# Kernel tuning notes

Measured on AMD Instinct MI355X. Metric: run time of the kernel, lower is better.

The kernel has to match this reference:

```python
import jax, jax.numpy as jnp
import numpy as np

NUM_HEADS = 8
NUM_KV_HEADS = 2
PATCH = 16
STRIDE = 8
HORIZON = 96
NQ = 3
EPS_RMS = 1e-6
EPS_REVIN = 1e-5


def rms_norm(x, scale):
    return x * jax.lax.rsqrt(jnp.mean(x * x, axis=-1, keepdims=True) + EPS_RMS) * scale


def lstm_scan(xs, wi, wh, b):
    # xs: (N, T, Din); flax OptimizedLSTMCell gate order i, f, g, o
    N = xs.shape[0]
    H = wh.shape[0]

    def step(carry, x_t):
        c, h = carry
        z = x_t @ wi + h @ wh + b
        i, f, g, o = jnp.split(z, 4, axis=-1)
        c = jax.nn.sigmoid(f) * c + jax.nn.sigmoid(i) * jnp.tanh(g)
        h = jax.nn.sigmoid(o) * jnp.tanh(c)
        return (c, h), h

    init = (jnp.zeros((N, H), xs.dtype), jnp.zeros((N, H), xs.dtype))
    _, hs = jax.lax.scan(step, init, jnp.swapaxes(xs, 0, 1))
    return jnp.swapaxes(hs, 0, 1)  # (N, T, H)


def gqa(x, wq, wk, wv, wo):
    # x: (B, S, D); non-causal grouped-query attention
    B, S, D = x.shape
    hd = wq.shape[1] // NUM_HEADS
    q = (x @ wq).reshape(B, S, NUM_HEADS, hd)
    k = (x @ wk).reshape(B, S, NUM_KV_HEADS, hd)
    v = (x @ wv).reshape(B, S, NUM_KV_HEADS, hd)
    rep = NUM_HEADS // NUM_KV_HEADS
    k = jnp.repeat(k, rep, axis=2)
    v = jnp.repeat(v, rep, axis=2)
    scale = jnp.asarray(1.0 / np.sqrt(hd), x.dtype)
    attn = jax.nn.softmax(jnp.einsum('bqhd,bkhd->bhqk', q, k) * scale, axis=-1)
    out = jnp.einsum('bhqk,bkhd->bqhd', attn, v).reshape(B, S, NUM_HEADS * hd)
    return out @ wo, attn


def setup_inputs() -> dict:
    key = jax.random.key(0)
    ks = jax.random.split(key, 12)
    b, d, m, T = 8, 16, 8, 512
    H, H2 = 256, 512
    NB = 4

    def w(k, shape, fan_in):
        return jax.random.normal(k, shape, jnp.float32) / np.sqrt(fan_in)

    return {
        'series': jax.random.normal(ks[0], (b, d, m, T), jnp.float32),
        'revin_scale': jnp.ones((m,), jnp.float32),
        'revin_bias': jnp.zeros((m,), jnp.float32),
        'up_w': w(ks[1], (PATCH, H), PATCH),
        'lstm_wi': w(ks[2], (NB, H, 4 * H2), H),
        'lstm_wh': w(ks[3], (NB, H2, 4 * H2), H2),
        'lstm_b': jnp.zeros((NB, 4 * H2), jnp.float32),
        'norm_scale': jnp.ones((NB, H2), jnp.float32),
        'wq': w(ks[4], (NB, H2, H2), H2),
        'wk': w(ks[5], (NB, H2, H2 // 4), H2),
        'wv': w(ks[6], (NB, H2, H2 // 4), H2),
        'wo': w(ks[7], (NB, H2, H2), H2),
        'down_w': w(ks[8], (NB, H2, H), H2),
        'head_norm_scale': jnp.ones((H,), jnp.float32),
        'point_w': w(ks[9], (H, HORIZON), H),
        'quant_w': w(ks[10], (H, HORIZON * NQ), H),
    }


def reference(series, revin_scale, revin_bias, up_w, lstm_wi, lstm_wh, lstm_b,
              norm_scale, wq, wk, wv, wo, down_w, head_norm_scale, point_w, quant_w):
    b, d, m, T = series.shape
    num_blocks = lstm_wi.shape[0]
    H = up_w.shape[1]
    H2 = lstm_wh.shape[1]

    # RevIN instance norm over time with per-metric affine
    mean = series.mean(axis=-1, keepdims=True)
    std = jnp.sqrt(series.var(axis=-1, keepdims=True) + EPS_REVIN)
    sc = revin_scale[:, None]
    bi = revin_bias[:, None]
    normed = (series - mean) / std * sc + bi

    # Patcher (seq_len=512, patch=16, stride=8 -> 63 patches, no padding needed)
    n_p = (T - PATCH) // STRIDE + 1
    idx = jnp.arange(n_p)[:, None] * STRIDE + jnp.arange(PATCH)
    patches = normed[..., idx]            # (b, d, m, np, ps)
    x = patches @ up_w                    # (b, d, m, np, H)

    for blk in range(num_blocks):
        s = x.reshape(b * d * m, n_p, H)
        hs = lstm_scan(s, lstm_wi[blk], lstm_wh[blk], lstm_b[blk])  # (bdm, np, H2)
        # '(b d m) np h -> (b m np) d h'
        hs = hs.reshape(b, d, m, n_p, H2).transpose(0, 2, 3, 1, 4).reshape(b * m * n_p, d, H2)
        nrm = rms_norm(hs, norm_scale[blk])
        mix, _ = gqa(nrm, wq[blk], wk[blk], wv[blk], wo[blk])
        bel = mix @ down_w[blk]           # (bmnp, d, H)
        # '(b m np) d h -> b d m np h'
        x = bel.reshape(b, m, n_p, d, H).transpose(0, 3, 1, 2, 4)

    # pooling_mode == 'last' with device mixer: last block's belief at last patch
    last = x[:, :, :, -1, :]              # (b, d, m, H)
    nb = rms_norm(last, head_norm_scale)
    point = nb @ point_w                  # (b, d, m, horizon)
    quant = (nb @ quant_w).reshape(b, d, m, HORIZON, NQ).transpose(4, 0, 1, 2, 3)

    def denorm(y):
        return (y - bi) / sc * std + mean

    point_u = denorm(point)
    quant_u = denorm(quant)               # broadcasts over leading quantile axis
    return jnp.concatenate([point_u[None], quant_u], axis=0)  # (1+NQ, b, d, m, horizon)
```

## Files before the change

### kernel.cpp

```cpp
#include <hip/hip_runtime.h>
#include <hip/hip_bf16.h>

#define NP 63

typedef __attribute__((ext_vector_type(8))) short short8;
typedef __attribute__((ext_vector_type(4))) float f32x4;
typedef __attribute__((ext_vector_type(4))) int i32x4;
typedef unsigned char uchar;

__device__ __forceinline__ float sigf(float x){ return 1.0f/(1.0f+expf(-x)); }
__device__ __forceinline__ float u2f(ushort u){ __hip_bfloat16 h; *(ushort*)&h = u; return __bfloat162float(h); }
__device__ __forceinline__ ushort f2u(float f){ __hip_bfloat16 h = __float2bfloat16(f); return *(ushort*)&h; }

__global__ void __launch_bounds__(256) k_revin(const float* __restrict__ series,
    float* __restrict__ meanv, float* __restrict__ stdv, int* __restrict__ bar)
{
  int n = blockIdx.x, tid = threadIdx.x;
  if(n==0 && tid<64) bar[tid] = 0;
  __shared__ float s1[256], s2[256];
  const float* p = series + n*512;
  float a = 0.f, b = 0.f;
  for(int t=tid;t<512;t+=256){ float v=p[t]; a+=v; b+=v*v; }
  s1[tid]=a; s2[tid]=b; __syncthreads();
  for(int s=128;s>0;s>>=1){
    if(tid<s){ s1[tid]+=s1[tid+s]; s2[tid]+=s2[tid+s]; }
    __syncthreads();
  }
  if(tid==0){
    float mu = s1[0]*(1.f/512.f);
    float var = fmaxf(s2[0]*(1.f/512.f) - mu*mu, 0.f);
    meanv[n]=mu; stdv[n]=sqrtf(var+1e-5f);
  }
}

__global__ void __launch_bounds__(256) k_patch(const float* __restrict__ series,
    const float* __restrict__ rs, const float* __restrict__ rb,
    const float* __restrict__ up_w, const float* __restrict__ meanv,
    const float* __restrict__ stdv, ushort* __restrict__ x)
{
  int n = blockIdx.x, tid = threadIdx.x;
  int m = n & 7;
  __shared__ float sn[512];
  float mu = meanv[n], sd = stdv[n];
  float A = rs[m]/sd, C = rb[m] - mu*A;
  const float* p = series + n*512;
  for(int t=tid;t<512;t+=256) sn[t] = p[t]*A + C;
  __syncthreads();
  float w[16];
  #pragma unroll
  for(int i=0;i<16;i++) w[i] = up_w[i*256+tid];
  ushort* xo = x + n*(NP*256);
  for(int pi=0;pi<NP;pi++){
    float acc=0.f;
    #pragma unroll
    for(int i=0;i<16;i++) acc = fmaf(sn[pi*8+i], w[i], acc);
    xo[pi*256+tid] = f2u(acc);
  }
}

__global__ void __launch_bounds__(256) k_wod(const float* __restrict__ wo,
    const float* __restrict__ dw, float* __restrict__ wod)
{
  int i = blockIdx.x, blk = blockIdx.y, tid = threadIdx.x;
  __shared__ float row[512];
  const float* wr = wo + (blk*512 + i)*512;
  for(int k=tid;k<512;k+=256) row[k]=wr[k];
  __syncthreads();
  const float* d = dw + blk*512*256;
  float acc=0.f;
  for(int k=0;k<512;k++) acc = fmaf(row[k], d[k*256+tid], acc);
  wod[(blk*512+i)*256+tid]=acc;
}

__global__ void __launch_bounds__(256) k_tr_wodt(const float* __restrict__ wod, ushort* __restrict__ wodt)
{
  __shared__ float tile[32][33];
  int blk = blockIdx.z;
  int n0 = blockIdx.x*32, k0 = blockIdx.y*32;
  int tid = threadIdx.x;
  #pragma unroll
  for(int i=0;i<4;i++){
    int idx = tid + 256*i; int kl = idx>>5, nl = idx&31;
    tile[kl][nl] = wod[blk*512*256 + (k0+kl)*256 + n0+nl];
  }
  __syncthreads();
  #pragma unroll
  for(int i=0;i<4;i++){
    int idx = tid + 256*i; int nl = idx>>5, kl = idx&31;
    wodt[blk*256*512 + (n0+nl)*512 + k0+kl] = f2u(tile[kl][nl]);
  }
}

__global__ void __launch_bounds__(256) k_tr_lstmw(const float* __restrict__ wi,
    const float* __restrict__ wh, ushort* __restrict__ wt)
{
  __shared__ float tile[32][33];
  int blk = blockIdx.z;
  int n0 = blockIdx.x*32, k0 = blockIdx.y*32;
  int tid = threadIdx.x;
  #pragma unroll
  for(int i=0;i<4;i++){
    int idx = tid + 256*i; int kl = idx>>5, nl = idx&31;
    int k = k0+kl, n = n0+nl;
    float v = (k<256) ? wi[blk*256*2048 + k*2048 + n]
                      : wh[blk*512*2048 + (k-256)*2048 + n];
    tile[kl][nl] = v;
  }
  __syncthreads();
  #pragma unroll
  for(int i=0;i<4;i++){
    int idx = tid + 256*i; int nl = idx>>5, kl = idx&31;
    wt[blk*2048*768 + (n0+nl)*768 + k0+kl] = f2u(tile[kl][nl]);
  }
}

__global__ void __launch_bounds__(256) k_tr_qkvw(const float* __restrict__ wq,
    const float* __restrict__ wk, const float* __restrict__ wv,
    const float* __restrict__ ns, ushort* __restrict__ wqkvt)
{
  __shared__ float tile[32][33];
  int blk = blockIdx.z;
  int n0 = blockIdx.x*32, k0 = blockIdx.y*32;
  int tid = threadIdx.x;
  #pragma unroll
  for(int i=0;i<4;i++){
    int idx = tid + 256*i; int kl = idx>>5, nl = idx&31;
    int k = k0+kl, n = n0+nl;
    float v;
    if(n < 512)      v = wq[blk*512*512 + k*512 + n];
    else if(n < 640) v = wk[blk*512*128 + k*128 + (n-512)];
    else             v = wv[blk*512*128 + k*128 + (n-640)];
    tile[kl][nl] = v * ns[blk*512 + k];
  }
  __syncthreads();
  #pragma unroll
  for(int i=0;i<4;i++){
    int idx = tid + 256*i; int nl = idx>>5, kl = idx&31;
    wqkvt[blk*768*512 + (n0+nl)*512 + k0+kl] = f2u(tile[kl][nl]);
  }
}

__global__ void __launch_bounds__(256,1) k_lstm_scan(
    const ushort* __restrict__ x, ushort* __restrict__ hs,
    const ushort* __restrict__ wt, const float* __restrict__ bias,
    uchar* __restrict__ flags, int tagbase)
{
  __shared__ __align__(16) short Bwh[128*512];
  __shared__ __align__(16) ushort hstage[64*32];
  int fb = blockIdx.x;
  int g = (fb & 7) | ((fb >> 4) & 8);
  int y = (fb >> 3) & 15;
  int n0 = g*64, jj0 = y*32;
  int tid = threadIdx.x;
  int wv = tid>>6, lane = tid&63, quad = lane>>4, l16 = lane&15;
  int wrow = wv>>1, wcol = wv&1;

  for(int i=tid; i<8192; i+=256){
    int c = i>>6, kb = i&63;
    short8 v = *(const short8*)(wt + ((c>>5)*512 + jj0 + (c&31))*768 + 256 + kb*8);
    *(short8*)((char*)Bwh + c*1024 + ((kb*16) ^ ((c&7)<<4))) = v;
  }
  int jj = jj0 + wcol*16 + l16;
  short8 bwi[4][8];
  #pragma unroll
  for(int gg=0; gg<4; gg++){
    const ushort* wp = wt + (gg*512 + jj)*768 + quad*8;
    #pragma unroll
    for(int ck=0; ck<8; ck++) bwi[gg][ck] = *(const short8*)(wp + ck*32);
  }
  float bI=bias[jj], bF=bias[512+jj], bG=bias[1024+jj], bO=bias[1536+jj];
  float cs[2][4];
  #pragma unroll
  for(int a=0;a<2;a++){
    #pragma unroll
    for(int r=0;r<4;r++) cs[a][r]=0.f;
  }
  const ushort* xb0 = x  + (n0 + wrow*32 + l16)*(NP*256) + quad*8;
  const ushort* hb0 = hs + (n0 + wrow*32 + l16)*(NP*512) + quad*8;
  int xorb = (l16&7)<<4;
  uchar* myflag = flags + g*16 + y;
  const uchar* gflags = flags + g*16;
  __syncthreads();

  for(int t=0; t<NP; ++t){
    f32x4 acc[4][2];
    #pragma unroll
    for(int gg=0; gg<4; gg++){ acc[gg][0]=(f32x4){0.f,0.f,0.f,0.f}; acc[gg][1]=(f32x4){0.f,0.f,0.f,0.f}; }

    #pragma unroll
    for(int ck=0; ck<8; ck++){
      short8 a0 = *(const short8*)(xb0 + t*256 + ck*32);
      short8 a1 = *(const short8*)(xb0 + 16*(NP*256) + t*256 + ck*32);
      #pragma unroll
      for(int gg=0; gg<4; gg++){
        acc[gg][0] = __builtin_amdgcn_mfma_f32_16x16x32_bf16(a0, bwi[gg][ck], acc[gg][0], 0,0,0);
        acc[gg][1] = __builtin_amdgcn_mfma_f32_16x16x32_bf16(a1, bwi[gg][ck], acc[gg][1], 0,0,0);
      }
    }

    if(t > 0){
      if(tid==0){
        uint tag = (uint)(tagbase + t);
        while(1){
          i32x4 f;
          asm volatile("global_load_dwordx4 %0, %1, off sc0 sc1\n\ts_waitcnt vmcnt(0)"
                       : "=&v"(f) : "v"(gflags) : "memory");
          uint ok = 1u;
          #pragma unroll
          for(int q=0;q<4;q++){
            uint w = (uint)f[q];
            if(( w      &0xffu) < tag) ok=0;
            if(((w>>8 ) &0xffu) < tag) ok=0;
            if(((w>>16) &0xffu) < tag) ok=0;
            if( (w>>24)         < tag) ok=0;
          }
          if(ok) break;
          __builtin_amdgcn_s_sleep(1);
        }
      }
      __syncthreads();

      const ushort* hb = hb0 + (t-1)*512;
      #pragma unroll
      for(int ck=0; ck<16; ck++){
        short8 a0 = *(const short8*)(hb + ck*32);
        short8 a1 = *(const short8*)(hb + 16*(NP*512) + ck*32);
        #pragma unroll
        for(int gg=0; gg<4; gg++){
          int c = gg*32 + wcol*16 + l16;
          short8 bh = *(short8*)((char*)Bwh + c*1024 + ((ck*64 + quad*16) ^ xorb));
          acc[gg][0] = __builtin_amdgcn_mfma_f32_16x16x32_bf16(a0, bh, acc[gg][0], 0,0,0);
          acc[gg][1] = __builtin_amdgcn_mfma_f32_16x16x32_bf16(a1, bh, acc[gg][1], 0,0,0);
        }
      }
    }

    #pragma unroll
    for(int a=0;a<2;a++){
      #pragma unroll
      for(int r=0;r<4;r++){
        int rowl = wrow*32 + a*16 + quad*4 + r;
        float zi=acc[0][a][r]+bI, zf=acc[1][a][r]+bF, zg=acc[2][a][r]+bG, zo=acc[3][a][r]+bO;
        float c = sigf(zf)*cs[a][r] + sigf(zi)*tanhf(zg);
        cs[a][r] = c;
        float hv = sigf(zo)*tanhf(c);
        int coll = wcol*16 + l16;
        int off = rowl*64 + ((coll*2) ^ (((rowl>>2)&3)<<4));
        *(ushort*)((char*)hstage + off) = f2u(hv);
      }
    }
    __syncthreads();
    {
      int rowl = tid>>2, c0b = (tid&3)*16;
      int off = rowl*64 + (c0b ^ (((rowl>>2)&3)<<4));
      i32x4 vv = *(const i32x4*)((const char*)hstage + off);
      ushort* gp = hs + ((size_t)(n0+rowl)*NP + t)*512 + jj0 + (tid&3)*8;
      asm volatile("global_store_dwordx4 %0, %1, off sc0 sc1" :: "v"(gp), "v"(vv) : "memory");
    }
    __syncthreads();
    if(tid==0 && t < NP-1){
      uint v = (uint)(tagbase + t + 1);
      asm volatile("global_store_byte %0, %1, off sc0 sc1" :: "v"(myflag), "v"(v) : "memory");
    }
  }
}

__global__ void __launch_bounds__(256) k_rms(const ushort* __restrict__ hs, float* __restrict__ rmsi)
{
  int tid = threadIdx.x;
  int r = blockIdx.x*4 + (tid>>6);
  int lane = tid&63;
  int bq = r/8064; int rr = r - bq*8064;
  int m = rr/1008; int rem = rr - m*1008;
  int p = rem>>4; int d = rem&15;
  int n = (bq*16+d)*8+m;
  const ushort* hp = hs + (n*NP+p)*512;
  float s=0.f;
  for(int c=lane;c<512;c+=64){ float v=u2f(hp[c]); s += v*v; }
  #pragma unroll
  for(int off=32;off>0;off>>=1) s += __shfl_down(s,off);
  if(lane==0) rmsi[r] = rsqrtf(s*(1.f/512.f)+1e-6f);
}

__global__ void __launch_bounds__(256) k_qkv_m(
    const ushort* __restrict__ hs, const float* __restrict__ rmsi,
    const ushort* __restrict__ wqkvt, ushort* __restrict__ qkv)
{
  __shared__ short As[64*40];
  __shared__ short Bs[128*40];
  int tid = threadIdx.x;
  int r0 = blockIdx.x*64, c0 = blockIdx.y*128;
  int wv = tid>>6, lane = tid&63, quad = lane>>4, l16 = lane&15;
  int arow = tid>>2, akp = tid&3;
  int r = r0 + arow;
  int bq = r/8064; int rr = r - bq*8064;
  int m = rr/1008; int rem = rr - m*1008;
  int p = rem>>4; int d = rem&15;
  int n = (bq*16+d)*8+m;
  const ushort* aptr = hs + (n*NP+p)*512 + akp*8;
  f32x4 acc[2][4];
  #pragma unroll
  for(int b=0;b<2;b++){
    #pragma unroll
    for(int a=0;a<4;a++) acc[b][a] = (f32x4){0.f,0.f,0.f,0.f};
  }
  for(int k0=0;k0<512;k0+=32){
    *(short8*)&As[arow*40+akp*8] = *(const short8*)(aptr + k0);
    #pragma unroll
    for(int i=0;i<2;i++){
      int pc = tid + 256*i; int rl=pc>>2, kp=pc&3;
      *(short8*)&Bs[rl*40+kp*8] = *(const short8*)(wqkvt + (c0+rl)*512 + k0 + kp*8);
    }
    __syncthreads();
    short8 af[4], bfr[2];
    #pragma unroll
    for(int a=0;a<4;a++) af[a] = *(short8*)&As[(a*16+l16)*40 + quad*8];
    #pragma unroll
    for(int b=0;b<2;b++) bfr[b] = *(short8*)&Bs[(wv*32+b*16+l16)*40 + quad*8];
    #pragma unroll
    for(int b=0;b<2;b++){
      #pragma unroll
      for(int a=0;a<4;a++)
        acc[b][a] = __builtin_amdgcn_mfma_f32_16x16x32_bf16(af[a], bfr[b], acc[b][a], 0,0,0);
    }
    __syncthreads();
  }
  #pragma unroll
  for(int a=0;a<4;a++){
    #pragma unroll
    for(int rg=0;rg<4;rg++){
      int rw = r0 + a*16 + quad*4 + rg;
      float rv = rmsi[rw];
      #pragma unroll
      for(int b=0;b<2;b++){
        int c = c0 + wv*32 + b*16 + l16;
        qkv[rw*768 + c] = f2u(acc[b][a][rg] * rv);
      }
    }
  }
}

__global__ void __launch_bounds__(256) k_attn(ushort* __restrict__ qkv)
{
  int r3 = blockIdx.x, h = blockIdx.y;
  int tid = threadIdx.x;
  __shared__ float qs[16][64];
  __shared__ float ks[16][65];
  __shared__ float vs[16][64];
  __shared__ float P[16][17];
  ushort* base = qkv + r3*16*768;
  int xx = tid&63, s4 = tid>>6;
  int kvh = (h>>2)*64;
  #pragma unroll
  for(int a=0;a<4;a++){
    int s = s4 + 4*a;
    qs[s][xx] = u2f(base[s*768 + h*64 + xx]);
    ks[s][xx] = u2f(base[s*768 + 512 + kvh + xx]);
    vs[s][xx] = u2f(base[s*768 + 640 + kvh + xx]);
  }
  __syncthreads();
  int i = tid>>4, j = tid&15;
  float sc = 0.f;
  #pragma unroll
  for(int xq=0;xq<64;xq++) sc = fmaf(qs[i][xq], ks[j][xq], sc);
  P[i][j] = sc*0.125f;
  __syncthreads();
  float row[16];
  #pragma unroll
  for(int jj=0;jj<16;jj++) row[jj] = P[i][jj];
  float mx = row[0];
  #pragma unroll
  for(int jj=1;jj<16;jj++) mx = fmaxf(mx, row[jj]);
  float sum = 0.f;
  #pragma unroll
  for(int jj=0;jj<16;jj++) sum += expf(row[jj]-mx);
  float pme = expf(row[j]-mx)/sum;
  __syncthreads();
  P[i][j] = pme;
  __syncthreads();
  #pragma unroll
  for(int a=0;a<4;a++){
    int s = s4 + 4*a;
    float o = 0.f;
    #pragma unroll
    for(int jj=0;jj<16;jj++) o = fmaf(P[s][jj], vs[jj][xx], o);
    base[s*768 + h*64 + xx] = f2u(o);
  }
}

__global__ void __launch_bounds__(256) k_bel_m(
    const ushort* __restrict__ qkv, const ushort* __restrict__ wodt,
    ushort* __restrict__ x)
{
  __shared__ short As[64*40];
  __shared__ short Bs[128*40];
  int tid = threadIdx.x;
  int r0 = blockIdx.x*64, c0 = blockIdx.y*128;
  int wv = tid>>6, lane = tid&63, quad = lane>>4, l16 = lane&15;
  int arow = tid>>2, akp = tid&3;
  const ushort* aptr = qkv + (r0+arow)*768 + akp*8;
  f32x4 acc[2][4];
  #pragma unroll
  for(int b=0;b<2;b++){
    #pragma unroll
    for(int a=0;a<4;a++) acc[b][a] = (f32x4){0.f,0.f,0.f,0.f};
  }
  for(int k0=0;k0<512;k0+=32){
    *(short8*)&As[arow*40+akp*8] = *(const short8*)(aptr + k0);
    #pragma unroll
    for(int i=0;i<2;i++){
      int pc = tid + 256*i; int rl=pc>>2, kp=pc&3;
      *(short8*)&Bs[rl*40+kp*8] = *(const short8*)(wodt + (c0+rl)*512 + k0 + kp*8);
    }
    __syncthreads();
    short8 af[4], bfr[2];
    #pragma unroll
    for(int a=0;a<4;a++) af[a] = *(short8*)&As[(a*16+l16)*40 + quad*8];
    #pragma unroll
    for(int b=0;b<2;b++) bfr[b] = *(short8*)&Bs[(wv*32+b*16+l16)*40 + quad*8];
    #pragma unroll
    for(int b=0;b<2;b++){
      #pragma unroll
      for(int a=0;a<4;a++)
        acc[b][a] = __builtin_amdgcn_mfma_f32_16x16x32_bf16(af[a], bfr[b], acc[b][a], 0,0,0);
    }
    __syncthreads();
  }
  #pragma unroll
  for(int a=0;a<4;a++){
    #pragma unroll
    for(int rg=0;rg<4;rg++){
      int rw = r0 + a*16 + quad*4 + rg;
      int bq = rw/8064; int rr = rw - bq*8064;
      int m = rr/1008; int rem = rr - m*1008;
      int p = rem>>4; int d = rem&15;
      int n = (bq*16+d)*8+m;
      ushort* xo = x + (n*NP+p)*256;
      #pragma unroll
      for(int b=0;b<2;b++){
        int c = c0 + wv*32 + b*16 + l16;
        xo[c] = f2u(acc[b][a][rg]);
      }
    }
  }
}

__global__ void __launch_bounds__(256) k_head(const ushort* __restrict__ x,
    const float* __restrict__ meanv, const float* __restrict__ stdv,
    const float* __restrict__ rs, const float* __restrict__ rb,
    const float* __restrict__ hns, const float* __restrict__ pw,
    const float* __restrict__ qw, float* __restrict__ out)
{
  int n = blockIdx.x, tid = threadIdx.x;
  __shared__ float nb[256];
  __shared__ float red[256];
  float v = u2f(x[(n*NP + 62)*256 + tid]);
  red[tid] = v*v; __syncthreads();
  for(int s=128;s>0;s>>=1){
    if(tid<s) red[tid]+=red[tid+s];
    __syncthreads();
  }
  float rinv = rsqrtf(red[0]*(1.f/256.f)+1e-6f);
  nb[tid] = v*rinv*hns[tid];
  __syncthreads();
  int m = n&7;
  float mu=meanv[n], sd=stdv[n], sc=rs[m], bi=rb[m];
  for(int col=tid; col<384; col+=256){
    float acc=0.f;
    int slot, hh;
    if(col < 96){
      for(int k=0;k<256;k++) acc = fmaf(nb[k], pw[k*96+col], acc);
      slot = 0; hh = col;
    } else {
      int cq = col-96;
      for(int k=0;k<256;k++) acc = fmaf(nb[k], qw[k*288+cq], acc);
      int qi = cq - (cq/3)*3;
      slot = 1 + qi; hh = cq/3;
    }
    float y = (acc - bi)/sc*sd + mu;
    out[(slot*1024 + n)*96 + hh] = y;
  }
}

extern "C" void kernel_launch(void* const* d_in, const int* in_sizes, int n_in,
                              void* d_out, int out_size, void* d_ws, size_t ws_size,
                              hipStream_t stream)
{
  const float* series    = (const float*)d_in[0];
  const float* rs        = (const float*)d_in[1];
  const float* rb        = (const float*)d_in[2];
  const float* up_w      = (const float*)d_in[3];
  const float* lstm_wi   = (const float*)d_in[4];
  const float* lstm_wh   = (const float*)d_in[5];
  const float* lstm_b    = (const float*)d_in[6];
  const float* norm_scale= (const float*)d_in[7];
  const float* wq        = (const float*)d_in[8];
  const float* wk        = (const float*)d_in[9];
  const float* wv        = (const float*)d_in[10];
  const float* wo        = (const float*)d_in[11];
  const float* down_w    = (const float*)d_in[12];
  const float* head_ns   = (const float*)d_in[13];
  const float* point_w   = (const float*)d_in[14];
  const float* quant_w   = (const float*)d_in[15];
  float* out = (float*)d_out;

  float* ws = (float*)d_ws;
  float*  meanv = ws;
  float*  stdv  = meanv + 1024;
  float*  rmsi  = stdv  + 1024;
  float*  cst   = rmsi  + 64512;
  float*  wodf  = cst   + 524288;
  ushort* xbuf  = (ushort*)(wodf + 524288);
  ushort* hsb   = xbuf  + 16515072;
  ushort* qkvb  = hsb   + 33030144;
  ushort* wt    = qkvb  + 49545216;
  ushort* wqkvt = wt    + 6291456;
  ushort* wodt  = wqkvt + 1572864;
  int*    bar   = (int*)cst;

  k_revin<<<1024,256,0,stream>>>(series, meanv, stdv, bar);
  k_patch<<<1024,256,0,stream>>>(series, rs, rb, up_w, meanv, stdv, xbuf);
  k_wod<<<dim3(512,4),256,0,stream>>>(wo, down_w, wodf);
  k_tr_wodt<<<dim3(8,16,4),256,0,stream>>>(wodf, wodt);
  k_tr_lstmw<<<dim3(64,24,4),256,0,stream>>>(lstm_wi, lstm_wh, wt);
  k_tr_qkvw<<<dim3(24,16,4),256,0,stream>>>(wq, wk, wv, norm_scale, wqkvt);

  for(int blk=0; blk<4; blk++){
    const ushort* wt_b = wt + blk*2048*768;
    const float*  bb   = lstm_b + blk*2048;
    k_lstm_scan<<<256,256,0,stream>>>(xbuf, hsb, wt_b, bb, (uchar*)bar, blk*NP);
    k_rms<<<16128,256,0,stream>>>(hsb, rmsi);
    k_qkv_m<<<dim3(1008,6),256,0,stream>>>(hsb, rmsi, wqkvt + blk*768*512, qkvb);
    k_attn<<<dim3(4032,8),256,0,stream>>>(qkvb);
    k_bel_m<<<dim3(1008,2),256,0,stream>>>(qkvb, wodt + blk*256*512, xbuf);
  }
  k_head<<<1024,256,0,stream>>>(xbuf, meanv, stdv, rs, rb, head_ns, point_w, quant_w, out);
}
```

Before: 3.818 ms.

## Use per-wave progress flags and per-chunk waits in LSTM scan

Replaces the block-wide barrier and single-thread spin in the persistent LSTM scan with per-wavefront flags: every wave publishes its own step counter, loads the group's flags before the input matmul, and waits only on the producer of each 32-column h chunk before consuming it. The LDS staging buffer and the two syncthreads per step are removed, and h values are written directly as scattered 2-byte global stores. Each block now gets its own flag region, so no tag offset is needed. The intent is to cut cross-block synchronization latency on the serial recurrence, at the cost of many more, smaller uncoalesced stores and more polling traffic.

```diff
diff --git a/kernel.cpp b/kernel.cpp
--- a/kernel.cpp
+++ b/kernel.cpp
@@ -12,11 +12,16 @@
 __device__ __forceinline__ float u2f(ushort u){ __hip_bfloat16 h; *(ushort*)&h = u; return __bfloat162float(h); }
 __device__ __forceinline__ ushort f2u(float f){ __hip_bfloat16 h = __float2bfloat16(f); return *(ushort*)&h; }
 
+__device__ __forceinline__ bool bytes_ok(uint d, uint tag){
+  return ((d & 0xffu) >= tag) & (((d>>8) & 0xffu) >= tag) &
+         (((d>>16) & 0xffu) >= tag) & ((d>>24) >= tag);
+}
+
 __global__ void __launch_bounds__(256) k_revin(const float* __restrict__ series,
     float* __restrict__ meanv, float* __restrict__ stdv, int* __restrict__ bar)
 {
   int n = blockIdx.x, tid = threadIdx.x;
-  if(n==0 && tid<64) bar[tid] = 0;
+  if(n==0){ for(int i=tid;i<1024;i+=256) bar[i]=0; }
   __shared__ float s1[256], s2[256];
   const float* p = series + n*512;
   float a = 0.f, b = 0.f;
@@ -143,10 +148,9 @@
 __global__ void __launch_bounds__(256,1) k_lstm_scan(
     const ushort* __restrict__ x, ushort* __restrict__ hs,
     const ushort* __restrict__ wt, const float* __restrict__ bias,
-    uchar* __restrict__ flags, int tagbase)
+    uchar* __restrict__ flags)
 {
   __shared__ __align__(16) short Bwh[128*512];
-  __shared__ __align__(16) ushort hstage[64*32];
   int fb = blockIdx.x;
   int g = (fb & 7) | ((fb >> 4) & 8);
   int y = (fb >> 3) & 15;
@@ -178,11 +182,19 @@
   const ushort* xb0 = x  + (n0 + wrow*32 + l16)*(NP*256) + quad*8;
   const ushort* hb0 = hs + (n0 + wrow*32 + l16)*(NP*512) + quad*8;
   int xorb = (l16&7)<<4;
-  uchar* myflag = flags + g*16 + y;
-  const uchar* gflags = flags + g*16;
+  const uchar* gflags = flags + g*64;
+  uchar* myflag = flags + g*64 + y*4 + wv;
   __syncthreads();
 
   for(int t=0; t<NP; ++t){
+    i32x4 f0, f1, f2, f3;
+    if(t > 0){
+      asm volatile("global_load_dwordx4 %0, %1, off sc0 sc1" : "=&v"(f0) : "v"(gflags)    );
+      asm volatile("global_load_dwordx4 %0, %1, off sc0 sc1" : "=&v"(f1) : "v"(gflags+16) );
+      asm volatile("global_load_dwordx4 %0, %1, off sc0 sc1" : "=&v"(f2) : "v"(gflags+32) );
+      asm volatile("global_load_dwordx4 %0, %1, off sc0 sc1" : "=&v"(f3) : "v"(gflags+48) );
+    }
+
     f32x4 acc[4][2];
     #pragma unroll
     for(int gg=0; gg<4; gg++){ acc[gg][0]=(f32x4){0.f,0.f,0.f,0.f}; acc[gg][1]=(f32x4){0.f,0.f,0.f,0.f}; }
@@ -199,68 +211,58 @@
     }
 
     if(t > 0){
-      if(tid==0){
-        uint tag = (uint)(tagbase + t);
-        while(1){
-          i32x4 f;
-          asm volatile("global_load_dwordx4 %0, %1, off sc0 sc1\n\ts_waitcnt vmcnt(0)"
-                       : "=&v"(f) : "v"(gflags) : "memory");
-          uint ok = 1u;
+      asm volatile("s_waitcnt vmcnt(0)" : "+v"(f0), "+v"(f1), "+v"(f2), "+v"(f3) :: "memory");
+      const ushort* hb = hb0 + (t-1)*512;
+      uint tag = (uint)t;
+      #pragma unroll
+      for(int yy=0; yy<16; yy++){
+        uint d;
+        if(yy<4)       d = (uint)f0[yy&3];
+        else if(yy<8)  d = (uint)f1[yy&3];
+        else if(yy<12) d = (uint)f2[yy&3];
+        else           d = (uint)f3[yy&3];
+        if(!bytes_ok(d, tag)){
+          const uchar* qa = gflags + (yy>>2)*16;
+          i32x4 fr;
+          do {
+            __builtin_amdgcn_s_sleep(1);
+            asm volatile("global_load_dwordx4 %0, %1, off sc0 sc1\n\ts_waitcnt vmcnt(0)"
+                         : "=&v"(fr) : "v"(qa) : "memory");
+            d = (uint)fr[yy&3];
+          } while(!bytes_ok(d, tag));
+        }
+        {
+          const int ck = yy;
+          short8 a0 = *(const short8*)(hb + ck*32);
+          short8 a1 = *(const short8*)(hb + 16*(NP*512) + ck*32);
           #pragma unroll
-          for(int q=0;q<4;q++){
-            uint w = (uint)f[q];
-            if(( w      &0xffu) < tag) ok=0;
-            if(((w>>8 ) &0xffu) < tag) ok=0;
-            if(((w>>16) &0xffu) < tag) ok=0;
-            if( (w>>24)         < tag) ok=0;
+          for(int gg=0; gg<4; gg++){
+            int c = gg*32 + wcol*16 + l16;
+            short8 bh = *(short8*)((char*)Bwh + c*1024 + ((ck*64 + quad*16) ^ xorb));
+            acc[gg][0] = __builtin_amdgcn_mfma_f32_16x16x32_bf16(a0, bh, acc[gg][0], 0,0,0);
+            acc[gg][1] = __builtin_amdgcn_mfma_f32_16x16x32_bf16(a1, bh, acc[gg][1], 0,0,0);
           }
-          if(ok) break;
-          __builtin_amdgcn_s_sleep(1);
         }
       }
-      __syncthreads();
-
-      const ushort* hb = hb0 + (t-1)*512;
-      #pragma unroll
-      for(int ck=0; ck<16; ck++){
-        short8 a0 = *(const short8*)(hb + ck*32);
-        short8 a1 = *(const short8*)(hb + 16*(NP*512) + ck*32);
-        #pragma unroll
-        for(int gg=0; gg<4; gg++){
-          int c = gg*32 + wcol*16 + l16;
-          short8 bh = *(short8*)((char*)Bwh + c*1024 + ((ck*64 + quad*16) ^ xorb));
-          acc[gg][0] = __builtin_amdgcn_mfma_f32_16x16x32_bf16(a0, bh, acc[gg][0], 0,0,0);
-          acc[gg][1] = __builtin_amdgcn_mfma_f32_16x16x32_bf16(a1, bh, acc[gg][1], 0,0,0);
-        }
-      }
     }
 
     #pragma unroll
     for(int a=0;a<2;a++){
       #pragma unroll
       for(int r=0;r<4;r++){
-        int rowl = wrow*32 + a*16 + quad*4 + r;
+        int n = n0 + wrow*32 + a*16 + quad*4 + r;
         float zi=acc[0][a][r]+bI, zf=acc[1][a][r]+bF, zg=acc[2][a][r]+bG, zo=acc[3][a][r]+bO;
         float c = sigf(zf)*cs[a][r] + sigf(zi)*tanhf(zg);
         cs[a][r] = c;
-        float hv = sigf(zo)*tanhf(c);
-        int coll = wcol*16 + l16;
-        int off = rowl*64 + ((coll*2) ^ (((rowl>>2)&3)<<4));
-        *(ushort*)((char*)hstage + off) = f2u(hv);
+        ushort hv = f2u(sigf(zo)*tanhf(c));
+        ushort* gp = hs + ((size_t)n*NP + t)*512 + jj;
+        asm volatile("global_store_short %0, %1, off sc0 sc1" :: "v"(gp), "v"(hv) : "memory");
       }
     }
-    __syncthreads();
-    {
-      int rowl = tid>>2, c0b = (tid&3)*16;
-      int off = rowl*64 + (c0b ^ (((rowl>>2)&3)<<4));
-      i32x4 vv = *(const i32x4*)((const char*)hstage + off);
-      ushort* gp = hs + ((size_t)(n0+rowl)*NP + t)*512 + jj0 + (tid&3)*8;
-      asm volatile("global_store_dwordx4 %0, %1, off sc0 sc1" :: "v"(gp), "v"(vv) : "memory");
-    }
-    __syncthreads();
-    if(tid==0 && t < NP-1){
-      uint v = (uint)(tagbase + t + 1);
-      asm volatile("global_store_byte %0, %1, off sc0 sc1" :: "v"(myflag), "v"(v) : "memory");
+    if(t < NP-1){
+      asm volatile("s_waitcnt vmcnt(0)" ::: "memory");
+      uint tv = (uint)(t+1);
+      asm volatile("global_store_byte %0, %1, off sc0 sc1" :: "v"(myflag), "v"(tv) : "memory");
     }
   }
 }
@@ -516,9 +518,9 @@
   ushort* wt    = qkvb  + 49545216;
   ushort* wqkvt = wt    + 6291456;
   ushort* wodt  = wqkvt + 1572864;
-  int*    bar   = (int*)cst;
-
-  k_revin<<<1024,256,0,stream>>>(series, meanv, stdv, bar);
+  uchar*  flagb = (uchar*)cst;
+
+  k_revin<<<1024,256,0,stream>>>(series, meanv, stdv, (int*)flagb);
   k_patch<<<1024,256,0,stream>>>(series, rs, rb, up_w, meanv, stdv, xbuf);
   k_wod<<<dim3(512,4),256,0,stream>>>(wo, down_w, wodf);
   k_tr_wodt<<<dim3(8,16,4),256,0,stream>>>(wodf, wodt);
@@ -528,7 +530,7 @@
   for(int blk=0; blk<4; blk++){
     const ushort* wt_b = wt + blk*2048*768;
     const float*  bb   = lstm_b + blk*2048;
-    k_lstm_scan<<<256,256,0,stream>>>(xbuf, hsb, wt_b, bb, (uchar*)bar, blk*NP);
+    k_lstm_scan<<<256,256,0,stream>>>(xbuf, hsb, wt_b, bb, flagb + blk*1024);
     k_rms<<<16128,256,0,stream>>>(hsb, rmsi);
     k_qkv_m<<<dim3(1008,6),256,0,stream>>>(hsb, rmsi, wqkvt + blk*768*512, qkvb);
     k_attn<<<dim3(4032,8),256,0,stream>>>(qkvb);
```

Measured after the change: 5.919 ms. 1.55x slower.
